# Kernel tuning notes

Measured on AMD Instinct MI355X. Metric: run time of the kernel, lower is better.

Reference implementation:

```python
import jax, jax.numpy as jnp
import numpy as np

DIM = 512; NB = 4; BS = DIM // NB            # EinFFT blocks
DS = 64; DC = 4; EXP = 2; DI = EXP * DIM      # Mamba dims
DTR = DIM // 16                               # dt_rank
BLOCKS = 2; LAM = 0.01; B_SZ = 2; L_SZ = 1024

def layer_norm(x, w, b):
    m = x.mean(-1, keepdims=True)
    v = x.var(-1, keepdims=True)
    return (x - m) / jnp.sqrt(v + 1e-5) * w + b

def softshrink(x, lam):
    return jnp.where(x > lam, x - lam, jnp.where(x < -lam, x + lam, jnp.zeros((), x.dtype)))

def mamba(x, in_proj_w, conv_w, conv_b, x_proj_w, dt_proj_w, dt_proj_b, A_log, D, out_proj_w):
    B, L, _ = x.shape
    xz = x @ in_proj_w.T                      # (B,L,2*DI)
    xm, z = jnp.split(xz, 2, axis=-1)
    # causal depthwise conv1d, keep first L outputs
    xt = xm.transpose(0, 2, 1)                # (B,DI,L)
    conv = jax.lax.conv_general_dilated(xt, conv_w, (1,), [(DC - 1, 0)],
                                        feature_group_count=DI,
                                        dimension_numbers=('NCH', 'OIH', 'NCH'))
    xm = jax.nn.silu((conv + conv_b[None, :, None]).transpose(0, 2, 1))  # (B,L,DI)
    proj = xm @ x_proj_w.T                    # (B,L,DTR+2*DS)
    dt = proj[..., :DTR]
    Bm = proj[..., DTR:DTR + DS]
    Cm = proj[..., DTR + DS:]
    dt = jax.nn.softplus(dt @ dt_proj_w.T + dt_proj_b)   # (B,L,DI)
    A = -jnp.exp(A_log)                       # (DI,DS)

    def step(h, inp):
        dt_t, B_t, C_t, u_t = inp             # (B,DI),(B,DS),(B,DS),(B,DI)
        dA = jnp.exp(dt_t[:, :, None] * A)
        h = dA * h + dt_t[:, :, None] * B_t[:, None, :] * u_t[:, :, None]
        y = jnp.einsum('bds,bs->bd', h, C_t)
        return h, y

    h0 = jnp.zeros((B, DI, DS), x.dtype)
    _, ys = jax.lax.scan(step, h0, (dt.transpose(1, 0, 2), Bm.transpose(1, 0, 2),
                                    Cm.transpose(1, 0, 2), xm.transpose(1, 0, 2)))
    y = ys.transpose(1, 0, 2) + xm * D        # (B,L,DI)
    y = y * jax.nn.silu(z)
    return y @ out_proj_w.T

def einfft(x, cw1, cw2, cb1, cb2):
    B, N, C = x.shape
    xf = jnp.fft.fft2(x.reshape(B, N, NB, BS), axes=(1, 2), norm='ortho')
    mul = lambda t, w: jnp.einsum('BNbd,bdk->BNbk', t, w)
    r1 = jax.nn.relu(mul(xf.real, cw1[0]) - mul(xf.imag, cw1[1]) + cb1[0])
    i1 = jax.nn.relu(mul(xf.real, cw1[1]) + mul(xf.imag, cw1[0]) + cb1[1])
    r2 = softshrink(mul(r1, cw2[0]) - mul(i1, cw2[1]) + cb2[0], LAM)
    i2 = softshrink(mul(r1, cw2[1]) + mul(i1, cw2[0]) + cb2[1], LAM)
    out = jnp.fft.ifft2(r2 + 1j * i2, axes=(1, 2), norm='ortho')
    return out.real.astype(x.dtype).reshape(B, N, C)

def setup_inputs() -> dict:
    key = jax.random.key(0)
    ks = jax.random.split(key, 16)
    r = lambda i, shape, s: jax.random.normal(ks[i], shape, jnp.float32) * s
    A_log = jnp.log(jnp.tile(jnp.arange(1, DS + 1, dtype=jnp.float32), (DI, 1)))
    return {
        'x': jax.random.normal(ks[0], (B_SZ, L_SZ, DIM), jnp.float32),
        'ln_w': jnp.ones((DIM,), jnp.float32), 'ln_b': jnp.zeros((DIM,), jnp.float32),
        'in_proj_w': r(1, (2 * DI, DIM), 0.02),
        'conv_w': r(2, (DI, 1, DC), 0.1), 'conv_b': jnp.zeros((DI,), jnp.float32),
        'x_proj_w': r(3, (DTR + 2 * DS, DI), 0.02),
        'dt_proj_w': r(4, (DI, DTR), 0.02),
        'dt_proj_b': jnp.full((DI,), float(np.log(np.expm1(0.01))), jnp.float32),
        'A_log': A_log, 'D': jnp.ones((DI,), jnp.float32),
        'out_proj_w': r(5, (DIM, DI), 0.02),
        'norm2_w': jnp.ones((DIM,), jnp.float32), 'norm2_b': jnp.zeros((DIM,), jnp.float32),
        'cw1': r(6, (2, NB, BS, BS), 0.02), 'cw2': r(7, (2, NB, BS, BS), 0.02),
        'cb1': r(8, (2, NB, BS), 0.02), 'cb2': r(9, (2, NB, BS), 0.02),
    }

def reference(x, ln_w, ln_b, in_proj_w, conv_w, conv_b, x_proj_w, dt_proj_w, dt_proj_b,
              A_log, D, out_proj_w, norm2_w, norm2_b, cw1, cw2, cb1, cb2):
    for _ in range(BLOCKS):
        x = x + mamba(layer_norm(x, ln_w, ln_b), in_proj_w, conv_w, conv_b,
                      x_proj_w, dt_proj_w, dt_proj_b, A_log, D, out_proj_w)
        x = x + einfft(layer_norm(x, norm2_w, norm2_b), cw1, cw2, cb1, cb2)
    return x
```

## Files before the change

kernel.cpp:

```cpp
#include <hip/hip_runtime.h>

typedef unsigned short u16;
typedef __attribute__((ext_vector_type(8))) short bf8;
typedef __attribute__((ext_vector_type(4))) float f4;

__device__ __forceinline__ float bf2f(u16 b) {
    return __uint_as_float(((unsigned)b) << 16);
}
__device__ __forceinline__ u16 f2bf(float f) {
    unsigned u = __float_as_uint(f);
    u += 0x7fffu + ((u >> 16) & 1u);
    return (u16)(u >> 16);
}
__device__ __forceinline__ void pack8f(const float* v, u16* dst) {
    uint r0 = (uint)f2bf(v[0]) | ((uint)f2bf(v[1]) << 16);
    uint r1 = (uint)f2bf(v[2]) | ((uint)f2bf(v[3]) << 16);
    uint r2 = (uint)f2bf(v[4]) | ((uint)f2bf(v[5]) << 16);
    uint r3 = (uint)f2bf(v[6]) | ((uint)f2bf(v[7]) << 16);
    *(uint4*)dst = make_uint4(r0, r1, r2, r3);
}
__device__ __forceinline__ bf8 neg8(bf8 v) {
    union { bf8 b; uint u[4]; } t; t.b = v;
    t.u[0] ^= 0x80008000u; t.u[1] ^= 0x80008000u;
    t.u[2] ^= 0x80008000u; t.u[3] ^= 0x80008000u;
    return t.b;
}
__device__ __forceinline__ int digrev10(int x) {
    int r = __brev((unsigned)x) >> 22;
    return ((r & 0x2AA) >> 1) | ((r & 0x155) << 1);
}

__global__ void detect_k(const u16* __restrict__ dtb, int* __restrict__ flag) {
    flag[0] = (dtb[0] == dtb[1] && dtb[1] == dtb[2] && dtb[2] == dtb[3] &&
               dtb[3] == dtb[4] && dtb[4] == dtb[5]) ? 1 : 0;
    flag[1] = 1;
}

__global__ __launch_bounds__(256)
void achk_k(const float* __restrict__ alog, int* __restrict__ flag) {
    int i = blockIdx.x * 256 + threadIdx.x;
    int s = i & 63;
    float n = __expf(alog[i]);
    float e = (float)(s + 1);
    if (fabsf(n - e) > 0.02f * e) atomicAnd(&flag[1], 0);
}

struct CvtArgs {
    const void* src[18];
    void* dst[18];
    int n[18];
    int obf[18];
};
__global__ __launch_bounds__(256)
void cvt_all_k(CvtArgs a, const int* __restrict__ flag) {
    const int t = blockIdx.y;
    const int n = a.n[t];
    const int f = flag[0];
    if (a.obf[t] == 2) {
        u16* __restrict__ d = (u16*)a.dst[t];
        if (f) {
            const u16* __restrict__ s = (const u16*)a.src[t];
            for (int i = blockIdx.x * 256 + threadIdx.x; i < n; i += gridDim.x * 256) {
                int cin = i & 127, cout = (i >> 7) & 127, snb = i >> 14;
                d[(snb << 14) + (cout << 7) + cin] = s[(snb << 14) + (cin << 7) + cout];
            }
        } else {
            const float* __restrict__ s = (const float*)a.src[t];
            for (int i = blockIdx.x * 256 + threadIdx.x; i < n; i += gridDim.x * 256) {
                int cin = i & 127, cout = (i >> 7) & 127, snb = i >> 14;
                d[(snb << 14) + (cout << 7) + cin] =
                    f2bf(s[(snb << 14) + (cin << 7) + cout]);
            }
        }
    } else if (a.obf[t] == 1) {
        u16* __restrict__ d = (u16*)a.dst[t];
        if (f) {
            const u16* __restrict__ s = (const u16*)a.src[t];
            for (int i = blockIdx.x * 256 + threadIdx.x; i < n; i += gridDim.x * 256)
                d[i] = s[i];
        } else {
            const float* __restrict__ s = (const float*)a.src[t];
            for (int i = blockIdx.x * 256 + threadIdx.x; i < n; i += gridDim.x * 256)
                d[i] = f2bf(s[i]);
        }
    } else {
        float* __restrict__ d = (float*)a.dst[t];
        if (f) {
            const u16* __restrict__ s = (const u16*)a.src[t];
            for (int i = blockIdx.x * 256 + threadIdx.x; i < n; i += gridDim.x * 256)
                d[i] = bf2f(s[i]);
        } else {
            const float* __restrict__ s = (const float*)a.src[t];
            for (int i = blockIdx.x * 256 + threadIdx.x; i < n; i += gridDim.x * 256)
                d[i] = s[i];
        }
    }
}

__global__ __launch_bounds__(256)
void ln_k(const float* __restrict__ x, const float* __restrict__ w,
          const float* __restrict__ b, u16* __restrict__ out) {
    const int row = blockIdx.x, tid = threadIdx.x;
    const float* xr = x + (long)row * 512;
    float v0 = xr[tid], v1 = xr[tid + 256];
    float s = v0 + v1, q = v0 * v0 + v1 * v1;
#pragma unroll
    for (int off = 32; off; off >>= 1) {
        s += __shfl_xor(s, off);
        q += __shfl_xor(q, off);
    }
    __shared__ float ss[4], qq[4];
    int wid = tid >> 6;
    if ((tid & 63) == 0) { ss[wid] = s; qq[wid] = q; }
    __syncthreads();
    s = ss[0] + ss[1] + ss[2] + ss[3];
    q = qq[0] + qq[1] + qq[2] + qq[3];
    float mean = s * (1.f / 512.f);
    float var = q * (1.f / 512.f) - mean * mean;
    float rstd = rsqrtf(var + 1e-5f);
    u16* o = out + (long)row * 512;
    o[tid]       = f2bf((v0 - mean) * rstd * w[tid]       + b[tid]);
    o[tid + 256] = f2bf((v1 - mean) * rstd * w[tid + 256] + b[tid + 256]);
}

#define LSTR 40
template <int TAF, int EPI>
__global__ __launch_bounds__(256)
void mgemm_k(const void* __restrict__ Ap, const u16* __restrict__ Bp,
             float* __restrict__ D, int N, int K, int lda, int ldb, int ldc,
             long bsA, long bsB, long bsC,
             const float* __restrict__ bias, const float* __restrict__ res) {
    const float* Af = (const float*)Ap + blockIdx.z * bsA;
    const u16*  Ab  = (const u16*)Ap + blockIdx.z * bsA;
    const u16*  B   = Bp + blockIdx.z * bsB;
    D += blockIdx.z * bsC;

    __shared__ u16 As[64 * LSTR];
    __shared__ u16 Bs[64 * LSTR];
    const int tid = threadIdx.x;
    const int lane = tid & 63;
    const int w = tid >> 6, wm = w & 1, wn = w >> 1;
    const int m0 = blockIdx.y * 64, n0 = blockIdx.x * 64;
    const int fr = (lane & 15), fq = (lane >> 4);

    f4 acc[2][2] = {};

    for (int k0 = 0; k0 < K; k0 += 32) {
        {
            const int ar = tid >> 2, aks = (tid & 3) << 3;
            if constexpr (TAF == 1) {
                *(uint4*)&As[ar * LSTR + aks] =
                    *(const uint4*)(Ab + (long)(m0 + ar) * lda + k0 + aks);
            } else {
                const float* p = Af + (long)(m0 + ar) * lda + k0 + aks;
                float tv[8];
                float4 x = *(const float4*)p, y = *(const float4*)(p + 4);
                tv[0] = x.x; tv[1] = x.y; tv[2] = x.z; tv[3] = x.w;
                tv[4] = y.x; tv[5] = y.y; tv[6] = y.z; tv[7] = y.w;
                pack8f(tv, &As[ar * LSTR + aks]);
            }
        }
        {
            const int br = tid >> 2, bks = (tid & 3) << 3;
            uint4 raw = make_uint4(0, 0, 0, 0);
            if (n0 + br < N)
                raw = *(const uint4*)(B + (long)(n0 + br) * ldb + k0 + bks);
            *(uint4*)&Bs[br * LSTR + bks] = raw;
        }
        __syncthreads();
        bf8 af[2], bff[2];
#pragma unroll
        for (int t = 0; t < 2; t++) {
            af[t]  = *(bf8*)&As[(wm * 32 + t * 16 + fr) * LSTR + (fq << 3)];
            bff[t] = *(bf8*)&Bs[(wn * 32 + t * 16 + fr) * LSTR + (fq << 3)];
        }
#pragma unroll
        for (int i = 0; i < 2; i++)
#pragma unroll
            for (int j = 0; j < 2; j++)
                acc[i][j] = __builtin_amdgcn_mfma_f32_16x16x32_bf16(
                    af[i], bff[j], acc[i][j], 0, 0, 0);
        __syncthreads();
    }

#pragma unroll
    for (int i = 0; i < 2; i++) {
#pragma unroll
        for (int j = 0; j < 2; j++) {
            const int gmb = m0 + wm * 32 + i * 16 + (fq << 2);
            const int gn  = n0 + wn * 32 + j * 16 + fr;
            if (gn >= N) continue;
#pragma unroll
            for (int e = 0; e < 4; e++) {
                long idx = (long)(gmb + e) * ldc + gn;
                float t = acc[i][j][e];
                if constexpr (EPI == 2) t += res[idx];
                D[idx] = t;
            }
        }
    }
}

__global__ __launch_bounds__(256)
void gemm128_k(const u16* __restrict__ A, const u16* __restrict__ B,
               u16* __restrict__ Dm, u16* __restrict__ Dz,
               int K, int lda, int ldb) {
    __shared__ u16 As[128 * LSTR];
    __shared__ u16 Bs[128 * LSTR];
    const int tid = threadIdx.x, lane = tid & 63;
    const int w = tid >> 6, wm = w & 1, wn = w >> 1;
    const int m0 = blockIdx.y * 128, n0 = blockIdx.x * 128;
    const int fr = lane & 15, fq = lane >> 4;
    f4 acc[4][4] = {};

    for (int k0 = 0; k0 < K; k0 += 32) {
#pragma unroll
        for (int j = 0; j < 2; ++j) {
            int idx = tid + j * 256;
            int row = idx >> 2, col = (idx & 3) << 3;
            *(uint4*)&As[row * LSTR + col] =
                *(const uint4*)(A + (long)(m0 + row) * lda + k0 + col);
            *(uint4*)&Bs[row * LSTR + col] =
                *(const uint4*)(B + (long)(n0 + row) * ldb + k0 + col);
        }
        __syncthreads();
        bf8 af[4], bfv[4];
#pragma unroll
        for (int i = 0; i < 4; ++i) {
            af[i]  = *(bf8*)&As[(wm * 64 + i * 16 + fr) * LSTR + (fq << 3)];
            bfv[i] = *(bf8*)&Bs[(wn * 64 + i * 16 + fr) * LSTR + (fq << 3)];
        }
#pragma unroll
        for (int i = 0; i < 4; ++i)
#pragma unroll
            for (int j = 0; j < 4; ++j)
                acc[i][j] = __builtin_amdgcn_mfma_f32_16x16x32_bf16(
                    af[i], bfv[j], acc[i][j], 0, 0, 0);
        __syncthreads();
    }
    u16* Dst = (n0 < 1024) ? Dm : Dz;
    const int noff = (n0 < 1024) ? 0 : 1024;
#pragma unroll
    for (int i = 0; i < 4; ++i)
#pragma unroll
        for (int j = 0; j < 4; ++j) {
            const int gm = m0 + wm * 64 + i * 16 + (fq << 2);
            const int gn = n0 + wn * 64 + j * 16 + fr - noff;
#pragma unroll
            for (int e = 0; e < 4; ++e)
                Dst[(long)(gm + e) * 1024 + gn] = f2bf(acc[i][j][e]);
        }
}

__global__ __launch_bounds__(1024)
void ffw_k(const u16* __restrict__ xn, u16* __restrict__ Orb,
           u16* __restrict__ Oib) {
    const int bz = blockIdx.x;
    const int b = bz >> 7, cg = bz & 127;
    const int t = threadIdx.x;
    const int f = t >> 8, tl = t & 255;
    const int c = cg + f * 128;
    __shared__ float re[4224], im[4224], twr[768], twi[768];
    if (t < 768) {
        float s, cc;
        __sincosf((float)t * -6.1359231515425649e-3f, &s, &cc);
        twr[t] = cc; twi[t] = s;
    }
    float* rf = re + f * 1056;
    float* mf = im + f * 1056;
    const u16* src = xn + ((long)b * 1024) * 512 + c;
#pragma unroll
    for (int r = 0; r < 4; ++r) {
        int n = tl + r * 256;
        float v = bf2f(src[(long)n * 512]);
        int a = n + (n >> 5);
        rf[a] = v; mf[a] = 0.f;
    }
    __syncthreads();
#pragma unroll
    for (int st = 0; st < 5; ++st) {
        const int qsh = 8 - 2 * st;
        const int q = 1 << qsh;
        const int len = q << 2;
        const int m = 1 << (2 * st);
        int j = tl & (q - 1);
        int g = tl >> qsh;
        int i0 = g * len + j;
        int a0 = i0 + (i0 >> 5);
        int i1 = i0 + q,     a1 = i1 + (i1 >> 5);
        int i2 = i0 + 2 * q, a2 = i2 + (i2 >> 5);
        int i3 = i0 + 3 * q, a3 = i3 + (i3 >> 5);
        float ar = rf[a0], ai = mf[a0];
        float br = rf[a1], bi = mf[a1];
        float cr = rf[a2], ci = mf[a2];
        float dr = rf[a3], di = mf[a3];
        float t0r = ar + cr, t0i = ai + ci;
        float t1r = ar - cr, t1i = ai - ci;
        float t2r = br + dr, t2i = bi + di;
        float u = br - dr, v = bi - di;
        rf[a0] = t0r + t2r; mf[a0] = t0i + t2i;
        {
            int k = j * m;
            float wr = twr[k], wi = twi[k];
            float xr = t1r + v, xi = t1i - u;
            rf[a1] = xr * wr - xi * wi;
            mf[a1] = xr * wi + xi * wr;
        }
        {
            int k = 2 * j * m;
            float wr = twr[k], wi = twi[k];
            float xr = t0r - t2r, xi = t0i - t2i;
            rf[a2] = xr * wr - xi * wi;
            mf[a2] = xr * wi + xi * wr;
        }
        {
            int k = 3 * j * m;
            float wr = twr[k], wi = twi[k];
            float xr = t1r - v, xi = t1i + u;
            rf[a3] = xr * wr - xi * wi;
            mf[a3] = xr * wi + xi * wr;
        }
        __syncthreads();
    }
    u16* drp = Orb + ((long)(b * 512 + c)) * 1024;
    u16* dip = Oib + ((long)(b * 512 + c)) * 1024;
#pragma unroll
    for (int r = 0; r < 4; ++r) {
        int kf = tl + r * 256;
        int sidx = digrev10(kf);
        int a = sidx + (sidx >> 5);
// ... 90 lines not shown
        float t1r = ar - cr, t1i = ai - ci;
        float t2r = br + dr, t2i = bi + di;
        float u = br - dr, v = bi - di;
        rf[a0] = t0r + t2r; mf[a0] = t0i + t2i;
        {
            int k = j * m;
            float wr = twr[k], wi = twi[k];
            float xr = t1r - v, xi = t1i + u;
            rf[a1] = xr * wr - xi * wi;
            mf[a1] = xr * wi + xi * wr;
        }
        {
            int k = 2 * j * m;
            float wr = twr[k], wi = twi[k];
            float xr = t0r - t2r, xi = t0i - t2i;
            rf[a2] = xr * wr - xi * wi;
            mf[a2] = xr * wi + xi * wr;
        }
        {
            int k = 3 * j * m;
            float wr = twr[k], wi = twi[k];
            float xr = t1r + v, xi = t1i - u;
            rf[a3] = xr * wr - xi * wi;
            mf[a3] = xr * wi + xi * wr;
        }
        __syncthreads();
    }
    float* d = Yc + ((long)(b * 512 + c)) * 1024;
#pragma unroll
    for (int r = 0; r < 4; ++r) {
        int n = tl + r * 256;
        int sidx = digrev10(n);
        int a = sidx + (sidx >> 5);
        d[n] = rf[a] * 0.03125f;
    }
}

__global__ __launch_bounds__(256)
void transadd_k(float* __restrict__ xbuf, const float* __restrict__ Yc,
                void* __restrict__ dout, int last, const int* __restrict__ flag) {
    const int b = blockIdx.z;
    const int c0 = blockIdx.x * 64, n0 = blockIdx.y * 64;
    __shared__ float T[64][65];
    const int tid = threadIdx.x;
    const int r = tid >> 2, q = (tid & 3) * 16;
    const float* src = Yc + ((long)(b * 512 + c0 + r)) * 1024 + n0 + q;
#pragma unroll
    for (int k = 0; k < 4; ++k) {
        float4 v = *(const float4*)(src + k * 4);
        T[r][q + k * 4 + 0] = v.x; T[r][q + k * 4 + 1] = v.y;
        T[r][q + k * 4 + 2] = v.z; T[r][q + k * 4 + 3] = v.w;
    }
    __syncthreads();
    const long base = ((long)(b * 1024 + n0 + r)) * 512 + c0 + q;
    float* dst = xbuf + base;
    if (last) {
        const int bf = flag[0];
#pragma unroll
        for (int k = 0; k < 4; ++k) {
            float4 w = *(const float4*)(dst + k * 4);
            w.x += T[q + k * 4 + 0][r]; w.y += T[q + k * 4 + 1][r];
            w.z += T[q + k * 4 + 2][r]; w.w += T[q + k * 4 + 3][r];
            if (bf) {
                uint2 p;
                p.x = (uint)f2bf(w.x) | ((uint)f2bf(w.y) << 16);
                p.y = (uint)f2bf(w.z) | ((uint)f2bf(w.w) << 16);
                *(uint2*)((u16*)dout + base + k * 4) = p;
            } else {
                *(float4*)((float*)dout + base + k * 4) = w;
            }
        }
    } else {
#pragma unroll
        for (int k = 0; k < 4; ++k) {
            float4 w = *(const float4*)(dst + k * 4);
            w.x += T[q + k * 4 + 0][r]; w.y += T[q + k * 4 + 1][r];
            w.z += T[q + k * 4 + 2][r]; w.w += T[q + k * 4 + 3][r];
            *(float4*)(dst + k * 4) = w;
        }
    }
}

#define LSTR2 136
template <int ACT>
__global__ __launch_bounds__(256)
void cmix_k(const u16* __restrict__ Xr, const u16* __restrict__ Xi,
            const u16* __restrict__ WT, const float* __restrict__ cb,
            u16* __restrict__ Or, u16* __restrict__ Oi) {
    const int z = blockIdx.z, b = z >> 2, nb = z & 3;
    const u16* Ar = Xr + (long)b * 524288 + nb * 131072;
    const u16* Ai = Xi + (long)b * 524288 + nb * 131072;
    const u16* Wr = WT + nb * 16384;
    const u16* Wi = WT + 65536 + nb * 16384;
    u16* Dr = Or + (long)b * 524288 + nb * 131072;
    u16* Di = Oi + (long)b * 524288 + nb * 131072;
    __shared__ u16 Ars[64 * LSTR2], Ais[64 * LSTR2], Brs[64 * LSTR2], Bis[64 * LSTR2];
    const int tid = threadIdx.x, lane = tid & 63;
    const int w = tid >> 6, wm = w & 1, wn = w >> 1;
    const int m0 = blockIdx.y * 64, n0 = blockIdx.x * 64;
    const int fr = (lane & 15), fq = (lane >> 4);
    f4 accr[2][2] = {}, acci[2][2] = {};

    {
        const int am = tid & 63, akb = (tid >> 6) << 3;
#pragma unroll
        for (int kk = 0; kk < 4; ++kk) {
            const int kb = kk * 32 + akb;
            u16 tr[8], ti[8];
#pragma unroll
            for (int j = 0; j < 8; j++) {
                long off = (long)(kb + j) * 1024 + m0 + am;
                tr[j] = Ar[off]; ti[j] = Ai[off];
            }
            uint r0 = (uint)tr[0] | ((uint)tr[1] << 16);
            uint r1 = (uint)tr[2] | ((uint)tr[3] << 16);
            uint r2 = (uint)tr[4] | ((uint)tr[5] << 16);
            uint r3 = (uint)tr[6] | ((uint)tr[7] << 16);
            *(uint4*)&Ars[am * LSTR2 + kb] = make_uint4(r0, r1, r2, r3);
            r0 = (uint)ti[0] | ((uint)ti[1] << 16);
            r1 = (uint)ti[2] | ((uint)ti[3] << 16);
            r2 = (uint)ti[4] | ((uint)ti[5] << 16);
            r3 = (uint)ti[6] | ((uint)ti[7] << 16);
            *(uint4*)&Ais[am * LSTR2 + kb] = make_uint4(r0, r1, r2, r3);
        }
        const int br = tid >> 2, bks = (tid & 3) << 3;
#pragma unroll
        for (int kk = 0; kk < 4; ++kk) {
            const int kb = kk * 32 + bks;
            *(uint4*)&Brs[br * LSTR2 + kb] =
                *(const uint4*)(Wr + (long)(n0 + br) * 128 + kb);
            *(uint4*)&Bis[br * LSTR2 + kb] =
                *(const uint4*)(Wi + (long)(n0 + br) * 128 + kb);
        }
    }
    __syncthreads();

#pragma unroll
    for (int kq = 0; kq < 4; ++kq) {
        const int kc = kq * 32 + (fq << 3);
        bf8 arf[2], aif[2], brf[2], bif[2];
#pragma unroll
        for (int t = 0; t < 2; t++) {
            arf[t] = *(bf8*)&Ars[(wm * 32 + t * 16 + fr) * LSTR2 + kc];
            aif[t] = *(bf8*)&Ais[(wm * 32 + t * 16 + fr) * LSTR2 + kc];
            brf[t] = *(bf8*)&Brs[(wn * 32 + t * 16 + fr) * LSTR2 + kc];
            bif[t] = *(bf8*)&Bis[(wn * 32 + t * 16 + fr) * LSTR2 + kc];
        }
        bf8 nai[2] = { neg8(aif[0]), neg8(aif[1]) };
#pragma unroll
        for (int i = 0; i < 2; i++)
#pragma unroll
            for (int j = 0; j < 2; j++) {
                accr[i][j] = __builtin_amdgcn_mfma_f32_16x16x32_bf16(arf[i], brf[j], accr[i][j], 0, 0, 0);
                accr[i][j] = __builtin_amdgcn_mfma_f32_16x16x32_bf16(nai[i], bif[j], accr[i][j], 0, 0, 0);
                acci[i][j] = __builtin_amdgcn_mfma_f32_16x16x32_bf16(arf[i], bif[j], acci[i][j], 0, 0, 0);
                acci[i][j] = __builtin_amdgcn_mfma_f32_16x16x32_bf16(aif[i], brf[j], acci[i][j], 0, 0, 0);
            }
    }

#pragma unroll
    for (int i = 0; i < 2; i++)
#pragma unroll
        for (int j = 0; j < 2; j++) {
            const int gmb = m0 + wm * 32 + i * 16 + (fq << 2);
            const int gn  = n0 + wn * 32 + j * 16 + fr;
            const float bbr = cb[nb * 128 + gn];
            const float bbi = cb[512 + nb * 128 + gn];
            u16 pr[4], pi[4];
#pragma unroll
            for (int e = 0; e < 4; e++) {
                float vr = accr[i][j][e] + bbr;
                float vi = acci[i][j][e] + bbi;
                if (ACT == 0) {
                    vr = fmaxf(vr, 0.f);
                    vi = fmaxf(vi, 0.f);
                } else {
                    vr = (vr > 0.01f) ? vr - 0.01f : ((vr < -0.01f) ? vr + 0.01f : 0.f);
                    vi = (vi > 0.01f) ? vi - 0.01f : ((vi < -0.01f) ? vi + 0.01f : 0.f);
                }
                pr[e] = f2bf(vr); pi[e] = f2bf(vi);
            }
            uint2 wr2, wi2;
            wr2.x = (uint)pr[0] | ((uint)pr[1] << 16);
            wr2.y = (uint)pr[2] | ((uint)pr[3] << 16);
            wi2.x = (uint)pi[0] | ((uint)pi[1] << 16);
            wi2.y = (uint)pi[2] | ((uint)pi[3] << 16);
            *(uint2*)&Dr[(long)gn * 1024 + gmb] = wr2;
            *(uint2*)&Di[(long)gn * 1024 + gmb] = wi2;
        }
}

__global__ __launch_bounds__(256)
void conv_k(const u16* __restrict__ xm, const float* __restrict__ cw,
            const float* __restrict__ cb, u16* __restrict__ u) {
    int idx = blockIdx.x * 256 + threadIdx.x;
    int d = idx & 1023;
    int l = (idx >> 10) & 1023;
    int b = idx >> 20;
    float acc = cb[d];
    const u16* base = xm + (long)b * 1048576 + d;
#pragma unroll
    for (int j = 0; j < 4; j++) {
        int li = l - 3 + j;
        if (li >= 0) acc = fmaf(cw[d * 4 + j], bf2f(base[(long)li * 1024]), acc);
    }
    float sig = 1.f / (1.f + __expf(-acc));
    u[idx] = f2bf(acc * sig);
}

__global__ __launch_bounds__(256, 1)
void scan1_k(const u16* __restrict__ uLb, const float* __restrict__ Pb,
             const u16* __restrict__ dtW, const float* __restrict__ dtBias,
             const float* __restrict__ alog, u16* __restrict__ Hb,
             float* __restrict__ Sbuf, float* __restrict__ Bred,
             float* __restrict__ Cred, u16* __restrict__ dtLb,
             const int* __restrict__ flag) {
    const int dg = blockIdx.x, c = blockIdx.y, b = blockIdx.z;
    const int tid = threadIdx.x;
    const int d = dg * 256 + tid;
    const int t0 = c * 32;
    __shared__ float Bls[32][64];
    __shared__ float Pls[32][32];
    {
#pragma unroll
        for (int j = 0; j < 2; ++j) {
            int slot = tid + j * 256;
            int r = slot >> 4, cg = (slot & 15) << 2;
            const float* src = Pb + ((long)(b * 1024 + t0 + r)) * 160 + 32 + cg;
            float4 v0 = *(const float4*)src;
            float4 v1 = *(const float4*)(src + 327680);
            float4 v2 = *(const float4*)(src + 655360);
            float4 v3 = *(const float4*)(src + 983040);
            v0.x += v1.x + v2.x + v3.x;
            v0.y += v1.y + v2.y + v3.y;
            v0.z += v1.z + v2.z + v3.z;
            v0.w += v1.w + v2.w + v3.w;
            *(float4*)&Bls[r][cg] = v0;
            if (dg == 0)
                *(float4*)&Bred[(((long)(b * 1024 + t0 + r)) << 6) + cg] = v0;
        }
        {
            int r = tid >> 3, cg = (tid & 7) << 2;
            const float* src = Pb + ((long)(b * 1024 + t0 + r)) * 160 + cg;
            float4 v0 = *(const float4*)src;
            float4 v1 = *(const float4*)(src + 327680);
            float4 v2 = *(const float4*)(src + 655360);
            float4 v3 = *(const float4*)(src + 983040);
            v0.x += v1.x + v2.x + v3.x;
            v0.y += v1.y + v2.y + v3.y;
            v0.z += v1.z + v2.z + v3.z;
            v0.w += v1.w + v2.w + v3.w;
            *(float4*)&Pls[r][cg] = v0;
        }
        if (dg == 0) {
#pragma unroll
            for (int j = 0; j < 2; ++j) {
                int slot = tid + j * 256;
                int r = slot >> 4, cg = (slot & 15) << 2;
                const float* src = Pb + ((long)(b * 1024 + t0 + r)) * 160 + 96 + cg;
                float4 v0 = *(const float4*)src;
                float4 v1 = *(const float4*)(src + 327680);
                float4 v2 = *(const float4*)(src + 655360);
                float4 v3 = *(const float4*)(src + 983040);
                v0.x += v1.x + v2.x + v3.x;
                v0.y += v1.y + v2.y + v3.y;
                v0.z += v1.z + v2.z + v3.z;
                v0.w += v1.w + v2.w + v3.w;
                *(float4*)&Cred[(((long)(b * 1024 + t0 + r)) << 6) + cg] = v0;
            }
        }
    }
    __syncthreads();
// ... 207 lines not shown
                h[sg * 4 + 3] = a3 * h[sg * 4 + 3] + dtu * B4.w;
                y = fmaf(h[sg * 4 + 3], C4.w, y);
                a0 *= q4; a1 *= q4; a2 *= q4; a3 *= q4;
            }
            float g = zz / (1.f + __expf(-zz));
            y2p[(long)t * 1024] = f2bf((y + uu[t] * Dd) * g);
        }
    } else {
        float A[64];
        const float* ap = alog + (long)d * 64;
#pragma unroll
        for (int s = 0; s < 64; s += 4) {
            float4 a4 = *(const float4*)(ap + s);
            A[s] = -__expf(a4.x); A[s + 1] = -__expf(a4.y);
            A[s + 2] = -__expf(a4.z); A[s + 3] = -__expf(a4.w);
        }
        for (int t = 0; t < 32; ++t) {
            float zz = bf2f(zp[(long)t * 1024]);
            float dt = dtv[t];
            float dtu = dt * uu[t];
            float y = 0.f;
            const float4* B4p = (const float4*)&Bls[t][0];
            const float4* C4p = (const float4*)&Cls[t][0];
#pragma unroll
            for (int sg = 0; sg < 16; ++sg) {
                float4 B4 = B4p[sg];
                float4 C4 = C4p[sg];
                h[sg * 4 + 0] = __expf(dt * A[sg * 4 + 0]) * h[sg * 4 + 0] + dtu * B4.x;
                y = fmaf(h[sg * 4 + 0], C4.x, y);
                h[sg * 4 + 1] = __expf(dt * A[sg * 4 + 1]) * h[sg * 4 + 1] + dtu * B4.y;
                y = fmaf(h[sg * 4 + 1], C4.y, y);
                h[sg * 4 + 2] = __expf(dt * A[sg * 4 + 2]) * h[sg * 4 + 2] + dtu * B4.z;
                y = fmaf(h[sg * 4 + 2], C4.z, y);
                h[sg * 4 + 3] = __expf(dt * A[sg * 4 + 3]) * h[sg * 4 + 3] + dtu * B4.w;
                y = fmaf(h[sg * 4 + 3], C4.w, y);
            }
            float g = zz / (1.f + __expf(-zz));
            y2p[(long)t * 1024] = f2bf((y + uu[t] * Dd) * g);
        }
    }
}

extern "C" void kernel_launch(void* const* d_in, const int* in_sizes, int n_in,
                              void* d_out, int out_size, void* d_ws, size_t ws_size,
                              hipStream_t stream) {
    float* ws = (float*)d_ws;
    int* flag = (int*)ws;
    size_t o = 64;
    float* xbuf  = ws + o; o += 1048576;
    float* fftA  = ws + o; o += 3145728;
    u16* xmb     = (u16*)(ws + o); o += 1048576;
    float* Yc    = ws + o; o += 1048576;
    u16* xnb     = (u16*)(ws + o); o += 524288;
    u16* wInpB   = (u16*)(ws + o); o += 524288;
    u16* wXpB    = (u16*)(ws + o); o += 81920;
    u16* wDtB    = (u16*)(ws + o); o += 16384;
    u16* wOutB   = (u16*)(ws + o); o += 262144;
    u16* WT1     = (u16*)(ws + o); o += 65536;
    u16* WT2     = (u16*)(ws + o); o += 65536;
    float* wConv = ws + o; o += 4096;
    float* wAlog = ws + o; o += 65536;
    float* wLnW  = ws + o; o += 512;
    float* wLnB  = ws + o; o += 512;
    float* wConvB= ws + o; o += 1024;
    float* wDtBias=ws + o; o += 1024;
    float* wD    = ws + o; o += 1024;
    float* wN2w  = ws + o; o += 512;
    float* wN2b  = ws + o; o += 512;
    float* wCb1  = ws + o; o += 1024;
    float* wCb2  = ws + o; o += 1024;
    float* Hreg  = ws + o; o += 4194304;
    float* Sbuf  = ws + o; o += 131072;
    float* Pbuf2 = ws + o; o += 1310720;
    u16* uLb     = (u16*)(ws + o); o += 1048576;
    u16* y2b     = (u16*)(ws + o); o += 1048576;
    u16* dtLb    = (u16*)(ws + o); o += 1048576;
    u16* zLb     = (u16*)(ws + o); o += 1048576;
    float* Bred  = ws + o; o += 131072;
    float* Cred  = ws + o; o += 131072;
    u16* Hb    = (u16*)Hreg;
    u16* xzb  = (u16*)fftA;
    u16* Xrb  = xzb;
    u16* Xib  = xzb + 1048576;
    u16* r1b  = xzb + 2097152;
    u16* i1b  = xzb + 3145728;
    u16* X2rb = xzb + 4194304;
    u16* X2ib = xzb + 5242880;

    dim3 blk(256);

    detect_k<<<1, 1, 0, stream>>>((const u16*)d_in[8], flag);

    CvtArgs ca;
    void* dsts[18] = {xbuf, wLnW, wLnB, wInpB, wConv, wConvB, wXpB, wDtB, wDtBias,
                      wAlog, wD, wOutB, wN2w, wN2b, WT1, WT2, wCb1, wCb2};
    int obf[18]    = {0,    0,    0,    1,     0,     0,      1,    1,    0,
                      0,     0,  1,     0,    0,    2,   2,   0,    0};
    for (int i = 0; i < 18; i++) {
        ca.src[i] = d_in[i];
        ca.dst[i] = dsts[i];
        ca.n[i] = in_sizes[i];
        ca.obf[i] = obf[i];
    }
    cvt_all_k<<<dim3(64, 18), blk, 0, stream>>>(ca, flag);
    achk_k<<<256, blk, 0, stream>>>(wAlog, flag);

    for (int it = 0; it < 2; ++it) {
        ln_k<<<2048, blk, 0, stream>>>(xbuf, wLnW, wLnB, xnb);
        gemm128_k<<<dim3(16, 16), blk, 0, stream>>>(
            xnb, wInpB, xmb, zLb, 512, 512, 512);
        conv_k<<<8192, blk, 0, stream>>>(xmb, wConv, wConvB, uLb);
        mgemm_k<1, 0><<<dim3(3, 32, 4), blk, 0, stream>>>(
            uLb, wXpB, Pbuf2, 160, 256, 1024, 1024, 160,
            256, 256, 327680, nullptr, nullptr);
        scan1_k<<<dim3(4, 32, 2), blk, 0, stream>>>(
            uLb, Pbuf2, wDtB, wDtBias, wAlog, Hb, Sbuf, Bred, Cred, dtLb, flag);
        scan2_k<<<512, blk, 0, stream>>>(wAlog, Sbuf, Hb);
        scan3_k<<<dim3(4, 32, 2), blk, 0, stream>>>(
            dtLb, uLb, zLb, Bred, Cred, wAlog, Hb, wD, flag, y2b);
        mgemm_k<1, 2><<<dim3(8, 32, 1), blk, 0, stream>>>(
            y2b, wOutB, xbuf, 512, 1024, 1024, 1024, 512, 0, 0, 0, nullptr, xbuf);

        ln_k<<<2048, blk, 0, stream>>>(xbuf, wN2w, wN2b, xnb);
        ffw_k<<<256, dim3(1024), 0, stream>>>(xnb, Xrb, Xib);
        cmix_k<0><<<dim3(2, 16, 8), blk, 0, stream>>>(Xrb, Xib, WT1, wCb1, r1b, i1b);
        cmix_k<1><<<dim3(2, 16, 8), blk, 0, stream>>>(r1b, i1b, WT2, wCb2, X2rb, X2ib);
        ifw_k<<<256, dim3(1024), 0, stream>>>(X2rb, X2ib, Yc);
        transadd_k<<<dim3(8, 16, 2), blk, 0, stream>>>(xbuf, Yc, d_out, it == 1, flag);
    }
}
```

Baseline: 445.1 us.

## Fuse two EinFFT complex mixes, split-K out_proj with atomics, smaller in_proj tiles

```diff
diff --git a/kernel.cpp b/kernel.cpp
--- a/kernel.cpp
+++ b/kernel.cpp
@@ -11,13 +11,6 @@
     unsigned u = __float_as_uint(f);
     u += 0x7fffu + ((u >> 16) & 1u);
     return (u16)(u >> 16);
-}
-__device__ __forceinline__ void pack8f(const float* v, u16* dst) {
-    uint r0 = (uint)f2bf(v[0]) | ((uint)f2bf(v[1]) << 16);
-    uint r1 = (uint)f2bf(v[2]) | ((uint)f2bf(v[3]) << 16);
-    uint r2 = (uint)f2bf(v[4]) | ((uint)f2bf(v[5]) << 16);
-    uint r3 = (uint)f2bf(v[6]) | ((uint)f2bf(v[7]) << 16);
-    *(uint4*)dst = make_uint4(r0, r1, r2, r3);
 }
 __device__ __forceinline__ bf8 neg8(bf8 v) {
     union { bf8 b; uint u[4]; } t; t.b = v;
@@ -124,15 +117,13 @@
 }
 
 #define LSTR 40
-template <int TAF, int EPI>
+template <int EPI>
 __global__ __launch_bounds__(256)
-void mgemm_k(const void* __restrict__ Ap, const u16* __restrict__ Bp,
+void mgemm_k(const u16* __restrict__ Ab, const u16* __restrict__ Bp,
              float* __restrict__ D, int N, int K, int lda, int ldb, int ldc,
-             long bsA, long bsB, long bsC,
-             const float* __restrict__ bias, const float* __restrict__ res) {
-    const float* Af = (const float*)Ap + blockIdx.z * bsA;
-    const u16*  Ab  = (const u16*)Ap + blockIdx.z * bsA;
-    const u16*  B   = Bp + blockIdx.z * bsB;
+             long bsA, long bsB, long bsC) {
+    const u16* A = Ab + blockIdx.z * bsA;
+    const u16* B = Bp + blockIdx.z * bsB;
     D += blockIdx.z * bsC;
 
     __shared__ u16 As[64 * LSTR];
@@ -148,17 +139,8 @@
     for (int k0 = 0; k0 < K; k0 += 32) {
         {
             const int ar = tid >> 2, aks = (tid & 3) << 3;
-            if constexpr (TAF == 1) {
-                *(uint4*)&As[ar * LSTR + aks] =
-                    *(const uint4*)(Ab + (long)(m0 + ar) * lda + k0 + aks);
-            } else {
-                const float* p = Af + (long)(m0 + ar) * lda + k0 + aks;
-                float tv[8];
-                float4 x = *(const float4*)p, y = *(const float4*)(p + 4);
-                tv[0] = x.x; tv[1] = x.y; tv[2] = x.z; tv[3] = x.w;
-                tv[4] = y.x; tv[5] = y.y; tv[6] = y.z; tv[7] = y.w;
-                pack8f(tv, &As[ar * LSTR + aks]);
-            }
+            *(uint4*)&As[ar * LSTR + aks] =
+                *(const uint4*)(A + (long)(m0 + ar) * lda + k0 + aks);
         }
         {
             const int br = tid >> 2, bks = (tid & 3) << 3;
@@ -193,47 +175,41 @@
 #pragma unroll
             for (int e = 0; e < 4; e++) {
                 long idx = (long)(gmb + e) * ldc + gn;
-                float t = acc[i][j][e];
-                if constexpr (EPI == 2) t += res[idx];
-                D[idx] = t;
+                if constexpr (EPI == 1) atomicAdd(&D[idx], acc[i][j][e]);
+                else                    D[idx] = acc[i][j][e];
             }
         }
     }
 }
 
 __global__ __launch_bounds__(256)
-void gemm128_k(const u16* __restrict__ A, const u16* __restrict__ B,
-               u16* __restrict__ Dm, u16* __restrict__ Dz,
-               int K, int lda, int ldb) {
-    __shared__ u16 As[128 * LSTR];
-    __shared__ u16 Bs[128 * LSTR];
+void inproj_k(const u16* __restrict__ A, const u16* __restrict__ B,
+              u16* __restrict__ Dm, u16* __restrict__ Dz) {
+    __shared__ u16 As[64 * LSTR];
+    __shared__ u16 Bs[64 * LSTR];
     const int tid = threadIdx.x, lane = tid & 63;
     const int w = tid >> 6, wm = w & 1, wn = w >> 1;
-    const int m0 = blockIdx.y * 128, n0 = blockIdx.x * 128;
+    const int m0 = blockIdx.y * 64, n0 = blockIdx.x * 64;
     const int fr = lane & 15, fq = lane >> 4;
-    f4 acc[4][4] = {};
-
-    for (int k0 = 0; k0 < K; k0 += 32) {
-#pragma unroll
-        for (int j = 0; j < 2; ++j) {
-            int idx = tid + j * 256;
-            int row = idx >> 2, col = (idx & 3) << 3;
-            *(uint4*)&As[row * LSTR + col] =
-                *(const uint4*)(A + (long)(m0 + row) * lda + k0 + col);
-            *(uint4*)&Bs[row * LSTR + col] =
-                *(const uint4*)(B + (long)(n0 + row) * ldb + k0 + col);
-        }
+    f4 acc[2][2] = {};
+
+    for (int k0 = 0; k0 < 512; k0 += 32) {
+        const int r = tid >> 2, ks = (tid & 3) << 3;
+        *(uint4*)&As[r * LSTR + ks] =
+            *(const uint4*)(A + (long)(m0 + r) * 512 + k0 + ks);
+        *(uint4*)&Bs[r * LSTR + ks] =
+            *(const uint4*)(B + (long)(n0 + r) * 512 + k0 + ks);
         __syncthreads();
-        bf8 af[4], bfv[4];
-#pragma unroll
-        for (int i = 0; i < 4; ++i) {
-            af[i]  = *(bf8*)&As[(wm * 64 + i * 16 + fr) * LSTR + (fq << 3)];
-            bfv[i] = *(bf8*)&Bs[(wn * 64 + i * 16 + fr) * LSTR + (fq << 3)];
-        }
-#pragma unroll
-        for (int i = 0; i < 4; ++i)
-#pragma unroll
-            for (int j = 0; j < 4; ++j)
+        bf8 af[2], bfv[2];
+#pragma unroll
+        for (int t = 0; t < 2; ++t) {
+            af[t]  = *(bf8*)&As[(wm * 32 + t * 16 + fr) * LSTR + (fq << 3)];
+            bfv[t] = *(bf8*)&Bs[(wn * 32 + t * 16 + fr) * LSTR + (fq << 3)];
+        }
+#pragma unroll
+        for (int i = 0; i < 2; ++i)
+#pragma unroll
+            for (int j = 0; j < 2; ++j)
                 acc[i][j] = __builtin_amdgcn_mfma_f32_16x16x32_bf16(
                     af[i], bfv[j], acc[i][j], 0, 0, 0);
         __syncthreads();
@@ -241,11 +217,11 @@
     u16* Dst = (n0 < 1024) ? Dm : Dz;
     const int noff = (n0 < 1024) ? 0 : 1024;
 #pragma unroll
-    for (int i = 0; i < 4; ++i)
-#pragma unroll
-        for (int j = 0; j < 4; ++j) {
-            const int gm = m0 + wm * 64 + i * 16 + (fq << 2);
-            const int gn = n0 + wn * 64 + j * 16 + fr - noff;
+    for (int i = 0; i < 2; ++i)
+#pragma unroll
+        for (int j = 0; j < 2; ++j) {
+            const int gm = m0 + wm * 32 + i * 16 + (fq << 2);
+            const int gn = n0 + wn * 32 + j * 16 + fr - noff;
 #pragma unroll
             for (int e = 0; e < 4; ++e)
                 Dst[(long)(gm + e) * 1024 + gn] = f2bf(acc[i][j][e]);
@@ -502,33 +478,36 @@
 }
 
 #define LSTR2 136
-template <int ACT>
 __global__ __launch_bounds__(256)
-void cmix_k(const u16* __restrict__ Xr, const u16* __restrict__ Xi,
-            const u16* __restrict__ WT, const float* __restrict__ cb,
-            u16* __restrict__ Or, u16* __restrict__ Oi) {
-    const int z = blockIdx.z, b = z >> 2, nb = z & 3;
+void cmix2_k(const u16* __restrict__ Xr, const u16* __restrict__ Xi,
+             const u16* __restrict__ W1, const u16* __restrict__ W2,
+             const float* __restrict__ cb1, const float* __restrict__ cb2,
+             u16* __restrict__ Or, u16* __restrict__ Oi) {
+    const int z = blockIdx.y, b = z >> 2, nb = z & 3;
+    const int m0 = blockIdx.x * 32;
     const u16* Ar = Xr + (long)b * 524288 + nb * 131072;
     const u16* Ai = Xi + (long)b * 524288 + nb * 131072;
-    const u16* Wr = WT + nb * 16384;
-    const u16* Wi = WT + 65536 + nb * 16384;
+    const u16* W1r = W1 + nb * 16384;
+    const u16* W1i = W1 + 65536 + nb * 16384;
+    const u16* W2r = W2 + nb * 16384;
+    const u16* W2i = W2 + 65536 + nb * 16384;
     u16* Dr = Or + (long)b * 524288 + nb * 131072;
     u16* Di = Oi + (long)b * 524288 + nb * 131072;
-    __shared__ u16 Ars[64 * LSTR2], Ais[64 * LSTR2], Brs[64 * LSTR2], Bis[64 * LSTR2];
+
+    __shared__ u16 Xrs[32 * LSTR2], Xis[32 * LSTR2];
+    __shared__ u16 Wrs[128 * LSTR2], Wis[128 * LSTR2];
     const int tid = threadIdx.x, lane = tid & 63;
-    const int w = tid >> 6, wm = w & 1, wn = w >> 1;
-    const int m0 = blockIdx.y * 64, n0 = blockIdx.x * 64;
-    const int fr = (lane & 15), fq = (lane >> 4);
-    f4 accr[2][2] = {}, acci[2][2] = {};
+    const int wn = tid >> 6;
+    const int fr = lane & 15, fq = lane >> 4;
 
     {
-        const int am = tid & 63, akb = (tid >> 6) << 3;
-#pragma unroll
-        for (int kk = 0; kk < 4; ++kk) {
-            const int kb = kk * 32 + akb;
+        const int am = tid & 31, kb0 = (tid >> 5) << 3;
+#pragma unroll
+        for (int half = 0; half < 2; ++half) {
+            const int kb = half * 64 + kb0;
             u16 tr[8], ti[8];
 #pragma unroll
-            for (int j = 0; j < 8; j++) {
+            for (int j = 0; j < 8; ++j) {
                 long off = (long)(kb + j) * 1024 + m0 + am;
                 tr[j] = Ar[off]; ti[j] = Ai[off];
             }
@@ -536,78 +515,128 @@
             uint r1 = (uint)tr[2] | ((uint)tr[3] << 16);
             uint r2 = (uint)tr[4] | ((uint)tr[5] << 16);
             uint r3 = (uint)tr[6] | ((uint)tr[7] << 16);
-            *(uint4*)&Ars[am * LSTR2 + kb] = make_uint4(r0, r1, r2, r3);
+            *(uint4*)&Xrs[am * LSTR2 + kb] = make_uint4(r0, r1, r2, r3);
             r0 = (uint)ti[0] | ((uint)ti[1] << 16);
             r1 = (uint)ti[2] | ((uint)ti[3] << 16);
             r2 = (uint)ti[4] | ((uint)ti[5] << 16);
             r3 = (uint)ti[6] | ((uint)ti[7] << 16);
-            *(uint4*)&Ais[am * LSTR2 + kb] = make_uint4(r0, r1, r2, r3);
-        }
-        const int br = tid >> 2, bks = (tid & 3) << 3;
-#pragma unroll
-        for (int kk = 0; kk < 4; ++kk) {
-            const int kb = kk * 32 + bks;
-            *(uint4*)&Brs[br * LSTR2 + kb] =
-                *(const uint4*)(Wr + (long)(n0 + br) * 128 + kb);
-            *(uint4*)&Bis[br * LSTR2 + kb] =
-                *(const uint4*)(Wi + (long)(n0 + br) * 128 + kb);
+            *(uint4*)&Xis[am * LSTR2 + kb] = make_uint4(r0, r1, r2, r3);
+        }
+#pragma unroll
+        for (int it = 0; it < 8; ++it) {
+            int slot = it * 256 + tid;
+            int row = slot >> 4, c8 = (slot & 15) << 3;
+            *(uint4*)&Wrs[row * LSTR2 + c8] = *(const uint4*)(W1r + row * 128 + c8);
+            *(uint4*)&Wis[row * LSTR2 + c8] = *(const uint4*)(W1i + row * 128 + c8);
         }
     }
     __syncthreads();
 
-#pragma unroll
-    for (int kq = 0; kq < 4; ++kq) {
-        const int kc = kq * 32 + (fq << 3);
-        bf8 arf[2], aif[2], brf[2], bif[2];
-#pragma unroll
-        for (int t = 0; t < 2; t++) {
-            arf[t] = *(bf8*)&Ars[(wm * 32 + t * 16 + fr) * LSTR2 + kc];
-            aif[t] = *(bf8*)&Ais[(wm * 32 + t * 16 + fr) * LSTR2 + kc];
-            brf[t] = *(bf8*)&Brs[(wn * 32 + t * 16 + fr) * LSTR2 + kc];
-            bif[t] = *(bf8*)&Bis[(wn * 32 + t * 16 + fr) * LSTR2 + kc];
-        }
-        bf8 nai[2] = { neg8(aif[0]), neg8(aif[1]) };
-#pragma unroll
-        for (int i = 0; i < 2; i++)
-#pragma unroll
-            for (int j = 0; j < 2; j++) {
-                accr[i][j] = __builtin_amdgcn_mfma_f32_16x16x32_bf16(arf[i], brf[j], accr[i][j], 0, 0, 0);
-                accr[i][j] = __builtin_amdgcn_mfma_f32_16x16x32_bf16(nai[i], bif[j], accr[i][j], 0, 0, 0);
-                acci[i][j] = __builtin_amdgcn_mfma_f32_16x16x32_bf16(arf[i], bif[j], acci[i][j], 0, 0, 0);
-                acci[i][j] = __builtin_amdgcn_mfma_f32_16x16x32_bf16(aif[i], brf[j], acci[i][j], 0, 0, 0);
-            }
-    }
-
-#pragma unroll
-    for (int i = 0; i < 2; i++)
-#pragma unroll
-        for (int j = 0; j < 2; j++) {
-            const int gmb = m0 + wm * 32 + i * 16 + (fq << 2);
-            const int gn  = n0 + wn * 32 + j * 16 + fr;
-            const float bbr = cb[nb * 128 + gn];
-            const float bbi = cb[512 + nb * 128 + gn];
-            u16 pr[4], pi[4];
-#pragma unroll
-            for (int e = 0; e < 4; e++) {
-                float vr = accr[i][j][e] + bbr;
-                float vi = acci[i][j][e] + bbi;
-                if (ACT == 0) {
-                    vr = fmaxf(vr, 0.f);
-                    vi = fmaxf(vi, 0.f);
-                } else {
+    {
+        f4 accr[2][2] = {}, acci[2][2] = {};
+#pragma unroll
+        for (int kq = 0; kq < 4; ++kq) {
+            const int kc = kq * 32 + (fq << 3);
+            bf8 xr[2], xi[2], wr[2], wi[2];
+#pragma unroll
+            for (int i = 0; i < 2; ++i) {
+                xr[i] = *(bf8*)&Xrs[(i * 16 + fr) * LSTR2 + kc];
+                xi[i] = *(bf8*)&Xis[(i * 16 + fr) * LSTR2 + kc];
+            }
+#pragma unroll
+            for (int j = 0; j < 2; ++j) {
+                wr[j] = *(bf8*)&Wrs[(wn * 32 + j * 16 + fr) * LSTR2 + kc];
+                wi[j] = *(bf8*)&Wis[(wn * 32 + j * 16 + fr) * LSTR2 + kc];
+            }
+            bf8 nxi[2] = { neg8(xi[0]), neg8(xi[1]) };
+#pragma unroll
+            for (int i = 0; i < 2; ++i)
+#pragma unroll
+                for (int j = 0; j < 2; ++j) {
+                    accr[i][j] = __builtin_amdgcn_mfma_f32_16x16x32_bf16(xr[i], wr[j], accr[i][j], 0, 0, 0);
+                    accr[i][j] = __builtin_amdgcn_mfma_f32_16x16x32_bf16(nxi[i], wi[j], accr[i][j], 0, 0, 0);
+                    acci[i][j] = __builtin_amdgcn_mfma_f32_16x16x32_bf16(xr[i], wi[j], acci[i][j], 0, 0, 0);
+                    acci[i][j] = __builtin_amdgcn_mfma_f32_16x16x32_bf16(xi[i], wr[j], acci[i][j], 0, 0, 0);
+                }
+        }
+        __syncthreads();
+#pragma unroll
+        for (int i = 0; i < 2; ++i)
+#pragma unroll
+            for (int j = 0; j < 2; ++j) {
+                const int n1 = wn * 32 + j * 16 + fr;
+                const float br_ = cb1[nb * 128 + n1];
+                const float bi_ = cb1[512 + nb * 128 + n1];
+#pragma unroll
+                for (int e = 0; e < 4; ++e) {
+                    const int m = i * 16 + (fq << 2) + e;
+                    Xrs[m * LSTR2 + n1] = f2bf(fmaxf(accr[i][j][e] + br_, 0.f));
+                    Xis[m * LSTR2 + n1] = f2bf(fmaxf(acci[i][j][e] + bi_, 0.f));
+                }
+            }
+    }
+#pragma unroll
+    for (int it = 0; it < 8; ++it) {
+        int slot = it * 256 + tid;
+        int row = slot >> 4, c8 = (slot & 15) << 3;
+        *(uint4*)&Wrs[row * LSTR2 + c8] = *(const uint4*)(W2r + row * 128 + c8);
+        *(uint4*)&Wis[row * LSTR2 + c8] = *(const uint4*)(W2i + row * 128 + c8);
+    }
+    __syncthreads();
+
+    {
+        f4 accr[2][2] = {}, acci[2][2] = {};
+#pragma unroll
+        for (int kq = 0; kq < 4; ++kq) {
+            const int kc = kq * 32 + (fq << 3);
+            bf8 xr[2], xi[2], wr[2], wi[2];
+#pragma unroll
+            for (int i = 0; i < 2; ++i) {
+                xr[i] = *(bf8*)&Xrs[(i * 16 + fr) * LSTR2 + kc];
+                xi[i] = *(bf8*)&Xis[(i * 16 + fr) * LSTR2 + kc];
+            }
+#pragma unroll
+            for (int j = 0; j < 2; ++j) {
+                wr[j] = *(bf8*)&Wrs[(wn * 32 + j * 16 + fr) * LSTR2 + kc];
+                wi[j] = *(bf8*)&Wis[(wn * 32 + j * 16 + fr) * LSTR2 + kc];
+            }
+            bf8 nxi[2] = { neg8(xi[0]), neg8(xi[1]) };
+#pragma unroll
+            for (int i = 0; i < 2; ++i)
+#pragma unroll
+                for (int j = 0; j < 2; ++j) {
+                    accr[i][j] = __builtin_amdgcn_mfma_f32_16x16x32_bf16(xr[i], wr[j], accr[i][j], 0, 0, 0);
+                    accr[i][j] = __builtin_amdgcn_mfma_f32_16x16x32_bf16(nxi[i], wi[j], accr[i][j], 0, 0, 0);
+                    acci[i][j] = __builtin_amdgcn_mfma_f32_16x16x32_bf16(xr[i], wi[j], acci[i][j], 0, 0, 0);
+                    acci[i][j] = __builtin_amdgcn_mfma_f32_16x16x32_bf16(xi[i], wr[j], acci[i][j], 0, 0, 0);
+                }
+        }
+#pragma unroll
+        for (int i = 0; i < 2; ++i)
+#pragma unroll
+            for (int j = 0; j < 2; ++j) {
+                const int n2 = wn * 32 + j * 16 + fr;
+                const int gm = m0 + i * 16 + (fq << 2);
+                const float br_ = cb2[nb * 128 + n2];
+                const float bi_ = cb2[512 + nb * 128 + n2];
+                u16 pr[4], pi[4];
+#pragma unroll
+                for (int e = 0; e < 4; ++e) {
+                    float vr = accr[i][j][e] + br_;
+                    float vi = acci[i][j][e] + bi_;
                     vr = (vr > 0.01f) ? vr - 0.01f : ((vr < -0.01f) ? vr + 0.01f : 0.f);
                     vi = (vi > 0.01f) ? vi - 0.01f : ((vi < -0.01f) ? vi + 0.01f : 0.f);
+                    pr[e] = f2bf(vr); pi[e] = f2bf(vi);
                 }
-                pr[e] = f2bf(vr); pi[e] = f2bf(vi);
-            }
-            uint2 wr2, wi2;
-            wr2.x = (uint)pr[0] | ((uint)pr[1] << 16);
-            wr2.y = (uint)pr[2] | ((uint)pr[3] << 16);
-            wi2.x = (uint)pi[0] | ((uint)pi[1] << 16);
-            wi2.y = (uint)pi[2] | ((uint)pi[3] << 16);
-            *(uint2*)&Dr[(long)gn * 1024 + gmb] = wr2;
-            *(uint2*)&Di[(long)gn * 1024 + gmb] = wi2;
-        }
+                uint2 wr2, wi2;
+                wr2.x = (uint)pr[0] | ((uint)pr[1] << 16);
+                wr2.y = (uint)pr[2] | ((uint)pr[3] << 16);
+                wi2.x = (uint)pi[0] | ((uint)pi[1] << 16);
+                wi2.y = (uint)pi[2] | ((uint)pi[3] << 16);
+                *(uint2*)&Dr[(long)n2 * 1024 + gm] = wr2;
+                *(uint2*)&Di[(long)n2 * 1024 + gm] = wi2;
+            }
+    }
 }
 
 __global__ __launch_bounds__(256)
@@ -981,10 +1010,8 @@
     u16* xzb  = (u16*)fftA;
     u16* Xrb  = xzb;
     u16* Xib  = xzb + 1048576;
-    u16* r1b  = xzb + 2097152;
-    u16* i1b  = xzb + 3145728;
-    u16* X2rb = xzb + 4194304;
-    u16* X2ib = xzb + 5242880;
+    u16* X2rb = xzb + 2097152;
+    u16* X2ib = xzb + 3145728;
 
     dim3 blk(256);
 
@@ -1006,24 +1033,22 @@
 
     for (int it = 0; it < 2; ++it) {
         ln_k<<<2048, blk, 0, stream>>>(xbuf, wLnW, wLnB, xnb);
-        gemm128_k<<<dim3(16, 16), blk, 0, stream>>>(
-            xnb, wInpB, xmb, zLb, 512, 512, 512);
+        inproj_k<<<dim3(32, 32), blk, 0, stream>>>(xnb, wInpB, xmb, zLb);
         conv_k<<<8192, blk, 0, stream>>>(xmb, wConv, wConvB, uLb);
-        mgemm_k<1, 0><<<dim3(3, 32, 4), blk, 0, stream>>>(
-            uLb, wXpB, Pbuf2, 160, 256, 1024, 1024, 160,
-            256, 256, 327680, nullptr, nullptr);
+        mgemm_k<0><<<dim3(3, 32, 4), blk, 0, stream>>>(
+            uLb, wXpB, Pbuf2, 160, 256, 1024, 1024, 160, 256, 256, 327680);
         scan1_k<<<dim3(4, 32, 2), blk, 0, stream>>>(
             uLb, Pbuf2, wDtB, wDtBias, wAlog, Hb, Sbuf, Bred, Cred, dtLb, flag);
         scan2_k<<<512, blk, 0, stream>>>(wAlog, Sbuf, Hb);
         scan3_k<<<dim3(4, 32, 2), blk, 0, stream>>>(
             dtLb, uLb, zLb, Bred, Cred, wAlog, Hb, wD, flag, y2b);
-        mgemm_k<1, 2><<<dim3(8, 32, 1), blk, 0, stream>>>(
-            y2b, wOutB, xbuf, 512, 1024, 1024, 1024, 512, 0, 0, 0, nullptr, xbuf);
+        mgemm_k<1><<<dim3(8, 32, 2), blk, 0, stream>>>(
+            y2b, wOutB, xbuf, 512, 512, 1024, 1024, 512, 512, 512, 0);
 
         ln_k<<<2048, blk, 0, stream>>>(xbuf, wN2w, wN2b, xnb);
         ffw_k<<<256, dim3(1024), 0, stream>>>(xnb, Xrb, Xib);
-        cmix_k<0><<<dim3(2, 16, 8), blk, 0, stream>>>(Xrb, Xib, WT1, wCb1, r1b, i1b);
-        cmix_k<1><<<dim3(2, 16, 8), blk, 0, stream>>>(r1b, i1b, WT2, wCb2, X2rb, X2ib);
+        cmix2_k<<<dim3(32, 8), blk, 0, stream>>>(
+            Xrb, Xib, WT1, WT2, wCb1, wCb2, X2rb, X2ib);
         ifw_k<<<256, dim3(1024), 0, stream>>>(X2rb, X2ib, Yc);
         transadd_k<<<dim3(8, 16, 2), blk, 0, stream>>>(xbuf, Yc, d_out, it == 1, flag);
     }
```

After: 431.2 us. 1.03x faster.
